# Performance work log

Measured on AMD Instinct MI355X. Metric: run time of the kernel, lower is better.

Reference implementation:

```python
import jax, jax.numpy as jnp
import numpy as np

QUERY_DIM = 1024
CONTEXT_DIM = 768
HEADS = 16
DIM_HEAD = 64
INNER = HEADS * DIM_HEAD  # 1024
SCALE = DIM_HEAD ** -0.5


def setup_inputs() -> dict:
    key = jax.random.key(0)
    ks = jax.random.split(key, 8)
    b, nq, nkv = 4, 2048, 1024
    x = jax.random.normal(ks[0], (b, nq, QUERY_DIM), dtype=jnp.float32)
    context = jax.random.normal(ks[1], (b, nkv, CONTEXT_DIM), dtype=jnp.float32)
    mask = jax.random.randint(ks[2], (b, nkv), 0, 2).astype(jnp.bool_)
    s = 0.02
    Wq = jax.random.normal(ks[3], (QUERY_DIM, INNER), dtype=jnp.float32) * s
    Wk = jax.random.normal(ks[4], (CONTEXT_DIM, INNER), dtype=jnp.float32) * s
    Wv = jax.random.normal(ks[5], (CONTEXT_DIM, INNER), dtype=jnp.float32) * s
    Wo = jax.random.normal(ks[6], (INNER, QUERY_DIM), dtype=jnp.float32) * s
    bo = jnp.zeros((QUERY_DIM,), dtype=jnp.float32)
    return {"x": x, "context": context, "mask": mask,
            "Wq": Wq, "Wk": Wk, "Wv": Wv, "Wo": Wo, "bo": bo}


def reference(x, context, mask, Wq, Wk, Wv, Wo, bo):
    b, nq, _ = x.shape
    nkv = context.shape[1]
    h, d = HEADS, DIM_HEAD
    # QKV projections (no bias, as in nn.Linear(..., bias=False))
    q = (x @ Wq).reshape(b, nq, h, d).transpose(0, 2, 1, 3)       # [b,h,i,d]
    k = (context @ Wk).reshape(b, nkv, h, d).transpose(0, 2, 1, 3)  # [b,h,j,d]
    v = (context @ Wv).reshape(b, nkv, h, d).transpose(0, 2, 1, 3)  # [b,h,j,d]
    sim = jnp.einsum('bhid,bhjd->bhij', q, k) * SCALE
    # mask is per-key [b, j]; broadcast over heads and query positions
    neg = jnp.finfo(sim.dtype).min
    sim = jnp.where(mask[:, None, None, :], sim, neg)
    attn = jax.nn.softmax(sim, axis=-1)
    out = jnp.einsum('bhij,bhjd->bhid', attn, v)                  # [b,h,i,d]
    out = out.transpose(0, 2, 1, 3).reshape(b, nq, h * d)          # [b,i,hd]
    return out @ Wo + bo
```

## Files before the change

kernel.cpp:

```cpp
#include <hip/hip_runtime.h>

typedef unsigned short u16;
typedef __attribute__((ext_vector_type(8))) __bf16 bf16x8;
typedef __attribute__((ext_vector_type(4))) float f32x4;
typedef __attribute__((ext_vector_type(16))) float f32x16;
typedef __attribute__((ext_vector_type(4))) u16 u16x4;

#define NB 4
#define NQ 2048
#define NKV 1024
#define NH 16
#define DH 64
#define DIN 1024
#define DCTX 768
#define NEGBIG -1e30f
#define QSC 0.180336881f

__device__ inline u16 f2bf(float f) {
  unsigned u = __builtin_bit_cast(unsigned, f);
  u += 0x7FFFu + ((u >> 16) & 1u);
  return (u16)(u >> 16);
}

__device__ inline unsigned cvtpk(float lo, float hi) {
  unsigned r;
  asm("v_cvt_pk_bf16_f32 %0, %1, %2" : "=v"(r) : "v"(lo), "v"(hi));
  return r;
}

__device__ inline float exp2a(float x) {
  float r;
  asm("v_exp_f32 %0, %1" : "=v"(r) : "v"(x));
  return r;
}

__global__ __launch_bounds__(256) void build_bias(const void* __restrict__ mask,
                                                  float* __restrict__ biasg) {
  __shared__ int notInt, notFloat;
  if (threadIdx.x == 0) { notInt = 0; notFloat = 0; }
  __syncthreads();
  const unsigned* mw = (const unsigned*)mask;
  int bad_i = 0, bad_f = 0;
#pragma unroll
  for (int e = 0; e < 4; e++) {
    unsigned v = mw[threadIdx.x * 4 + e];
    if (v > 1u) bad_i = 1;
    if (v != 0u && v != 0x3f800000u) bad_f = 1;
  }
  if (bad_i) atomicOr(&notInt, 1);
  if (bad_f) atomicOr(&notFloat, 1);
  __syncthreads();
  const int isInt = !notInt, isFloat = !notFloat;
  for (int i = threadIdx.x; i < NB * NKV; i += 256) {
    bool on;
    if (isInt)        on = ((const int*)mask)[i] != 0;
    else if (isFloat) on = ((const float*)mask)[i] != 0.f;
    else              on = ((const unsigned char*)mask)[i] != 0;
    biasg[i] = on ? 0.f : NEGBIG;
  }
}

__global__ __launch_bounds__(256) void cvt_bf16(const float* __restrict__ in,
                                                u16* __restrict__ out, int n) {
  int i = (blockIdx.x * 256 + threadIdx.x) * 4;
  if (i >= n) return;
  float4 v = *(const float4*)(in + i);
  u16x4 o = { f2bf(v.x), f2bf(v.y), f2bf(v.z), f2bf(v.w) };
  *(u16x4*)(out + i) = o;
}

__global__ __launch_bounds__(256) void transpose_cvt(const float* __restrict__ W,
                                                     u16* __restrict__ Wt, int K, int N) {
  __shared__ float tile[32][33];
  int n0 = blockIdx.x * 32, k0 = blockIdx.y * 32;
  int tx = threadIdx.x & 31, ty = threadIdx.x >> 5;
#pragma unroll
  for (int i = 0; i < 32; i += 8)
    tile[ty + i][tx] = W[(size_t)(k0 + ty + i) * N + n0 + tx];
  __syncthreads();
#pragma unroll
  for (int i = 0; i < 32; i += 8)
    Wt[(size_t)(n0 + ty + i) * K + k0 + tx] = f2bf(tile[tx][ty + i]);
}

__global__ __launch_bounds__(256) void vtrans(const u16* __restrict__ kvb, u16* __restrict__ vtg) {
  __shared__ __align__(16) u16 tile[64][72];
  const int t = threadIdx.x;
  const int jt = blockIdx.x, bh = blockIdx.y;
  const int b = bh >> 4, h = bh & 15;
  const int j0 = jt * 64;
  const int jl = t >> 2, c2 = t & 3;
  const u16* src = kvb + (size_t)(b * 1024 + j0 + jl) * 2048 + 1024 + h * 64 + c2 * 16;
  *(int4*)&tile[jl][c2 * 16]     = *(const int4*)(src);
  *(int4*)&tile[jl][c2 * 16 + 8] = *(const int4*)(src + 8);
  __syncthreads();
  const int dl = t >> 2;
  union { u16 e[16]; int4 q[2]; } pk;
#pragma unroll
  for (int e = 0; e < 16; e++) pk.e[e] = tile[c2 * 16 + e][dl];
  u16* dst = vtg + (size_t)(bh * 64 + dl) * 1024 + j0 + c2 * 16;
  *(int4*)dst       = pk.q[0];
  *(int4*)(dst + 8) = pk.q[1];
}

template<int MODE>
__global__ __launch_bounds__(256) void gemm_bt(const u16* __restrict__ A,
                                               const u16* __restrict__ Bt,
                                               void* __restrict__ Cout,
                                               const float* __restrict__ bias,
                                               int M, int N, int K) {
  __shared__ __align__(16) u16 As[2][128 * 32];
  __shared__ __align__(16) u16 Bs[2][128 * 32];
  const int t = threadIdx.x, w = t >> 6, l = t & 63, g = l >> 4, m16 = l & 15;
  const int brow = blockIdx.y * 128, bcol = blockIdx.x * 128;
  const int wr = w >> 1, wc = w & 1;
  const int r_a = t >> 2;
  const int kb  = (t & 3) * 8;
  const int nk = K >> 5;
  f32x4 acc[4][4] = {};

#define G_STAGE(ks, bsel)                                                              \
  {                                                                                    \
    int k0_ = (ks) << 5;                                                               \
    _Pragma("unroll")                                                                  \
    for (int i = 0; i < 2; i++) {                                                      \
      const u16* ga = A + (size_t)(brow + i * 64 + r_a) * K + k0_ + kb;                \
      __builtin_amdgcn_global_load_lds(                                                \
          (const __attribute__((address_space(1))) void*)ga,                           \
          (__attribute__((address_space(3))) void*)((char*)As + (bsel) * 8192 + i * 4096 + w * 1024), \
          16, 0, 0);                                                                   \
      const u16* gb = Bt + (size_t)(bcol + i * 64 + r_a) * K + k0_ + kb;               \
      __builtin_amdgcn_global_load_lds(                                                \
          (const __attribute__((address_space(1))) void*)gb,                           \
          (__attribute__((address_space(3))) void*)((char*)Bs + (bsel) * 8192 + i * 4096 + w * 1024), \
          16, 0, 0);                                                                   \
    }                                                                                  \
  }

  G_STAGE(0, 0);
  asm volatile("s_waitcnt vmcnt(0)" ::: "memory");
  __builtin_amdgcn_s_barrier();

  for (int ks = 0; ks < nk; ++ks) {
    const int cur = ks & 1;
    bf16x8 af[4], bfr[4];
#pragma unroll
    for (int m = 0; m < 4; m++)
      af[m] = *(const bf16x8*)(&As[cur][(wr * 64 + m * 16 + m16) * 32 + g * 8]);
#pragma unroll
    for (int n = 0; n < 4; n++)
      bfr[n] = *(const bf16x8*)(&Bs[cur][(wc * 64 + n * 16 + m16) * 32 + g * 8]);
    if (ks + 1 < nk) G_STAGE(ks + 1, cur ^ 1);
#pragma unroll
    for (int m = 0; m < 4; m++)
#pragma unroll
      for (int n = 0; n < 4; n++)
        acc[m][n] = __builtin_amdgcn_mfma_f32_16x16x32_bf16(af[m], bfr[n], acc[m][n], 0, 0, 0);
    asm volatile("s_waitcnt vmcnt(0)" ::: "memory");
    __builtin_amdgcn_s_barrier();
  }
#undef G_STAGE

#pragma unroll
  for (int m = 0; m < 4; m++) {
    int grow = brow + wr * 64 + m * 16 + g * 4;
#pragma unroll
    for (int n = 0; n < 4; n++) {
      int gcol = bcol + wc * 64 + n * 16 + m16;
#pragma unroll
      for (int r = 0; r < 4; r++) {
        size_t off = (size_t)(grow + r) * N + gcol;
        if (MODE == 0)      ((float*)Cout)[off] = acc[m][n][r] + bias[gcol];
        else if (MODE == 1) ((u16*)Cout)[off] = f2bf(acc[m][n][r]);
        else                ((u16*)Cout)[off] = f2bf(acc[m][n][r] * QSC);
      }
    }
  }
}

__global__ __launch_bounds__(256) void attn(const u16* __restrict__ Q, const u16* __restrict__ Kb,
                                            const u16* __restrict__ Vt_g,
                                            const float* __restrict__ biasg,
                                            u16* __restrict__ O) {
  const int qt = blockIdx.x, h = blockIdx.y, b = blockIdx.z;
  const int t = threadIdx.x, w = t >> 6, l = t & 63;
  const int i32 = l & 31, hi = l >> 5;
  const int bh = b * NH + h;

  __shared__ __align__(16) u16 Kl[2][4096];
  __shared__ __align__(16) u16 Vt[2][4096];
  __shared__ float biasl[NKV];

  for (int i = t; i < NKV; i += 256) biasl[i] = biasg[(size_t)b * NKV + i];

  const int qrow = qt * 128 + w * 32 + i32;
  const u16* qp = Q + (size_t)(b * NQ + qrow) * DIN + h * DH;
  bf16x8 qf[4];
#pragma unroll
  for (int c = 0; c < 4; c++) qf[c] = *(const bf16x8*)(qp + c * 16 + hi * 8);

  f32x16 oacc[2] = {};
  float lA = 0.f;

#define STAGE_K(j0, bsel)                                                     \
  {                                                                           \
    _Pragma("unroll")                                                         \
    for (int n = 0; n < 2; n++) {                                             \
      int j_ = n * 32 + (t >> 3);                                             \
      int c_ = (t & 7) ^ (j_ & 7);                                            \
      const u16* gk = Kb + (size_t)(b * NKV + (j0) + j_) * 2048 + h * DH + c_ * 8; \
      __builtin_amdgcn_global_load_lds(                                       \
          (const __attribute__((address_space(1))) void*)gk,                  \
          (__attribute__((address_space(3))) void*)((char*)Kl + (bsel) * 8192 + n * 4096 + t * 16), \
          16, 0, 0);                                                          \
    }                                                                         \
  }
#define STAGE_V(j0, bsel)                                                     \
  {                                                                           \
    _Pragma("unroll")                                                         \
    for (int n = 0; n < 2; n++) {                                             \
      int d_ = n * 32 + (t >> 3);                                             \
      int c_ = (t & 7) ^ (d_ & 7);                                            \
      const u16* gv = Vt_g + (size_t)(bh * 64 + d_) * 1024 + (j0) + c_ * 8;   \
      __builtin_amdgcn_global_load_lds(                                       \
          (const __attribute__((address_space(1))) void*)gv,                  \
          (__attribute__((address_space(3))) void*)((char*)Vt + (bsel) * 8192 + n * 4096 + t * 16), \
          16, 0, 0);                                                          \
    }                                                                         \
  }

  STAGE_K(0, 0);
  STAGE_V(0, 0);
  asm volatile("s_waitcnt vmcnt(0)" ::: "memory");
  __builtin_amdgcn_s_barrier();

  for (int it = 0; it < 16; ++it) {
    const int cur = it & 1, nxt = cur ^ 1;
    const int j0 = it * 64;
    if (it + 1 < 16) {
      STAGE_K(j0 + 64, nxt);
      STAGE_V(j0 + 64, nxt);
    }

    bf16x8 pa[4];
#pragma unroll
    for (int jt = 0; jt < 2; jt++) {
      f32x16 s = {};
#pragma unroll
      for (int c = 0; c < 4; c++) {
        bf16x8 kf = *(const bf16x8*)&Kl[cur][(jt * 32 + i32) * 64 + (((2 * c + hi) ^ (i32 & 7)) * 8)];
        s = __builtin_amdgcn_mfma_f32_32x32x16_bf16(kf, qf[c], s, 0, 0, 0);
      }
      float4 qb4[4];
#pragma unroll
      for (int a = 0; a < 4; a++)
        qb4[a] = *(const float4*)&biasl[j0 + jt * 32 + a * 8 + hi * 4];
      float p[16];
#pragma unroll
      for (int r = 0; r < 16; r++) {
        const float* bq = (const float*)&qb4[r >> 2];
        p[r] = exp2a(s[r] + bq[r & 3]);
      }
#pragma unroll
      for (int r = 0; r < 16; r += 4)
        lA += ((p[r] + p[r + 1]) + (p[r + 2] + p[r + 3]));
      unsigned u[4][2];
#pragma unroll
      for (int a = 0; a < 4; a++) {
        u[a][0] = cvtpk(p[4 * a], p[4 * a + 1]);
        u[a][1] = cvtpk(p[4 * a + 2], p[4 * a + 3]);
      }
#pragma unroll
      for (int cc = 0; cc < 2; cc++) {
        unsigned s0 = hi ? u[2 * cc][0] : u[2 * cc + 1][0];
        unsigned s1 = hi ? u[2 * cc][1] : u[2 * cc + 1][1];
        unsigned r0 = __shfl_xor(s0, 32);
        unsigned r1 = __shfl_xor(s1, 32);
        union { unsigned uu[4]; bf16x8 v; } pw;
        pw.uu[0] = hi ? r0 : u[2 * cc][0];
        pw.uu[1] = hi ? r1 : u[2 * cc][1];
        pw.uu[2] = hi ? u[2 * cc + 1][0] : r0;
        pw.uu[3] = hi ? u[2 * cc + 1][1] : r1;
        pa[jt * 2 + cc] = pw.v;
      }
    }
#pragma unroll
    for (int dt = 0; dt < 2; dt++) {
      const int d = dt * 32 + i32;
#pragma unroll
      for (int kc = 0; kc < 4; kc++) {
        bf16x8 vf = *(const bf16x8*)&Vt[cur][d * 64 + (((2 * kc + hi) ^ (i32 & 7)) * 8)];
        oacc[dt] = __builtin_amdgcn_mfma_f32_32x32x16_bf16(pa[kc], vf, oacc[dt], 0, 0, 0);
      }
    }
    asm volatile("s_waitcnt vmcnt(0)" ::: "memory");
    __builtin_amdgcn_s_barrier();
  }
#undef STAGE_K
#undef STAGE_V

  lA += __shfl_xor(lA, 32);
  float inv = 1.f / lA;
  u16* op = O + (size_t)(b * NQ + qt * 128 + w * 32) * DIN + h * DH;
#pragma unroll
  for (int reg = 0; reg < 16; reg++) {
    const int irow = (reg & 3) + 8 * (reg >> 2) + 4 * hi;
    const float iv = __shfl(inv, irow);
#pragma unroll
    for (int dt = 0; dt < 2; dt++)
      op[(size_t)irow * DIN + dt * 32 + i32] = f2bf(oacc[dt][reg] * iv);
  }
}

extern "C" void kernel_launch(void* const* d_in, const int* in_sizes, int n_in,
                              void* d_out, int out_size, void* d_ws, size_t ws_size,
                              hipStream_t stream) {
  const float* x   = (const float*)d_in[0];
  const float* ctx = (const float*)d_in[1];
  const void*  mask = (const void*)d_in[2];
  const float* Wq  = (const float*)d_in[3];
  const float* Wk  = (const float*)d_in[4];
  const float* Wv  = (const float*)d_in[5];
  const float* Wo  = (const float*)d_in[6];
  const float* bo  = (const float*)d_in[7];
  float* out = (float*)d_out;

  char* ws = (char*)d_ws;
  u16* xb   = (u16*)(ws);
  u16* cb   = (u16*)(ws + 16777216);
  u16* wqt  = (u16*)(ws + 23068672);
  u16* wkv  = (u16*)(ws + 25165824);
  u16* wot  = (u16*)(ws + 28311552);
  u16* qb   = (u16*)(ws + 30408704);
  u16* kvb  = (u16*)(ws + 47185920);
  u16* vtg  = (u16*)(ws + 16777216);
  float* biasg = (float*)(ws + 63963136);
  u16* ab   = xb;

  build_bias<<<1, 256, 0, stream>>>(mask, biasg);
  cvt_bf16<<<8192, 256, 0, stream>>>(x, xb, 8388608);
  cvt_bf16<<<3072, 256, 0, stream>>>(ctx, cb, 3145728);
  transpose_cvt<<<dim3(32, 32), 256, 0, stream>>>(Wq, wqt, 1024, 1024);
  transpose_cvt<<<dim3(32, 24), 256, 0, stream>>>(Wk, wkv, 768, 1024);
  transpose_cvt<<<dim3(32, 24), 256, 0, stream>>>(Wv, wkv + 1024 * 768, 768, 1024);
  transpose_cvt<<<dim3(32, 32), 256, 0, stream>>>(Wo, wot, 1024, 1024);

  gemm_bt<2><<<dim3(8, 64), 256, 0, stream>>>(xb, wqt, qb, nullptr, 8192, 1024, 1024);
  gemm_bt<1><<<dim3(16, 32), 256, 0, stream>>>(cb, wkv, kvb, nullptr, 4096, 2048, 768);

  vtrans<<<dim3(16, 64), 256, 0, stream>>>(kvb, vtg);

  attn<<<dim3(16, 16, 4), 256, 0, stream>>>(qb, kvb, vtg, biasg, ab);

  gemm_bt<0><<<dim3(8, 64), 256, 0, stream>>>(ab, wot, out, bo, 8192, 1024, 1024);
}
```

Measured before the change: 271.0 us.

## Rewrite projection GEMMs as 256x128 triple-buffered kernel; fold mask bias into MFMA init

The GEMM kernel moves to 256x128 tiles with 512 threads, K-step 64, an XOR-swizzled LDS layout and three-stage buffering with partial vmcnt waits, plus a block-index swizzle for L2 locality. In attention, the mask bias now initialises the MFMA accumulator, which removes the per-element add before exp. s_setprio raises wave priority around the MFMA blocks in both kernels. The larger tiles and three-deep buffers use much more LDS per block (144KB), which limits blocks per CU. The grid mapping hardcodes 256 blocks with an 8-way swizzle that assumes gx*gy=256.

```diff
diff --git a/kernel.cpp b/kernel.cpp
--- a/kernel.cpp
+++ b/kernel.cpp
@@ -104,69 +104,95 @@
 }
 
 template<int MODE>
-__global__ __launch_bounds__(256) void gemm_bt(const u16* __restrict__ A,
-                                               const u16* __restrict__ Bt,
-                                               void* __restrict__ Cout,
-                                               const float* __restrict__ bias,
-                                               int M, int N, int K) {
-  __shared__ __align__(16) u16 As[2][128 * 32];
-  __shared__ __align__(16) u16 Bs[2][128 * 32];
+__global__ __launch_bounds__(512) void gemm256p(const u16* __restrict__ A,
+                                                const u16* __restrict__ Bt,
+                                                void* __restrict__ Cout,
+                                                const float* __restrict__ bias,
+                                                int N, int K) {
+  __shared__ __align__(16) u16 As[3][256 * 64];
+  __shared__ __align__(16) u16 Bs[3][128 * 64];
   const int t = threadIdx.x, w = t >> 6, l = t & 63, g = l >> 4, m16 = l & 15;
-  const int brow = blockIdx.y * 128, bcol = blockIdx.x * 128;
-  const int wr = w >> 1, wc = w & 1;
-  const int r_a = t >> 2;
-  const int kb  = (t & 3) * 8;
-  const int nk = K >> 5;
+  const int gx = N >> 7;
+  const int bid = blockIdx.x;
+  const int sw = (bid & 7) * 32 + (bid >> 3);
+  const int bx = sw % gx, by = sw / gx;
+  const int brow = by * 256, bcol = bx * 128;
+  const int wm = w >> 1, wn = w & 1;
+  const int nk = K >> 6;
+  const int srow = t >> 3;
+  const int sc   = t & 7;
   f32x4 acc[4][4] = {};
 
-#define G_STAGE(ks, bsel)                                                              \
-  {                                                                                    \
-    int k0_ = (ks) << 5;                                                               \
-    _Pragma("unroll")                                                                  \
-    for (int i = 0; i < 2; i++) {                                                      \
-      const u16* ga = A + (size_t)(brow + i * 64 + r_a) * K + k0_ + kb;                \
-      __builtin_amdgcn_global_load_lds(                                                \
-          (const __attribute__((address_space(1))) void*)ga,                           \
-          (__attribute__((address_space(3))) void*)((char*)As + (bsel) * 8192 + i * 4096 + w * 1024), \
-          16, 0, 0);                                                                   \
-      const u16* gb = Bt + (size_t)(bcol + i * 64 + r_a) * K + k0_ + kb;               \
-      __builtin_amdgcn_global_load_lds(                                                \
-          (const __attribute__((address_space(1))) void*)gb,                           \
-          (__attribute__((address_space(3))) void*)((char*)Bs + (bsel) * 8192 + i * 4096 + w * 1024), \
-          16, 0, 0);                                                                   \
-    }                                                                                  \
-  }
-
-  G_STAGE(0, 0);
-  asm volatile("s_waitcnt vmcnt(0)" ::: "memory");
-  __builtin_amdgcn_s_barrier();
-
+#define STAGE(ks, bsel)                                                              \
+  {                                                                                  \
+    int k0_ = (ks) << 6;                                                             \
+    _Pragma("unroll")                                                                \
+    for (int r = 0; r < 4; r++) {                                                    \
+      int row = r * 64 + srow;                                                       \
+      int cs = sc ^ (row & 7);                                                       \
+      const u16* ga = A + (size_t)(brow + row) * K + k0_ + cs * 8;                   \
+      __builtin_amdgcn_global_load_lds(                                              \
+          (const __attribute__((address_space(1))) void*)ga,                         \
+          (__attribute__((address_space(3))) void*)((char*)As + (bsel) * 32768 + r * 8192 + t * 16), \
+          16, 0, 0);                                                                 \
+    }                                                                                \
+    _Pragma("unroll")                                                                \
+    for (int r = 0; r < 2; r++) {                                                    \
+      int row = r * 64 + srow;                                                       \
+      int cs = sc ^ (row & 7);                                                       \
+      const u16* gb = Bt + (size_t)(bcol + row) * K + k0_ + cs * 8;                  \
+      __builtin_amdgcn_global_load_lds(                                              \
+          (const __attribute__((address_space(1))) void*)gb,                         \
+          (__attribute__((address_space(3))) void*)((char*)Bs + (bsel) * 16384 + r * 8192 + t * 16), \
+          16, 0, 0);                                                                 \
+    }                                                                                \
+  }
+
+  STAGE(0, 0);
+  STAGE(1, 1);
+  int cur = 0;
   for (int ks = 0; ks < nk; ++ks) {
-    const int cur = ks & 1;
-    bf16x8 af[4], bfr[4];
+    if (ks + 1 < nk) asm volatile("s_waitcnt vmcnt(6)" ::: "memory");
+    else             asm volatile("s_waitcnt vmcnt(0)" ::: "memory");
+    __builtin_amdgcn_s_barrier();
+    if (ks + 2 < nk) {
+      const int stg = (cur >= 1) ? cur - 1 : 2;
+      STAGE(ks + 2, stg);
+    }
+    bf16x8 af[4][2], bfr[4][2];
+#pragma unroll
+    for (int m = 0; m < 4; m++) {
+      const int row = wm * 64 + m * 16 + m16;
+#pragma unroll
+      for (int kh = 0; kh < 2; kh++)
+        af[m][kh] = *(const bf16x8*)(&As[cur][row * 64 + (((kh * 4 + g) ^ (m16 & 7)) * 8)]);
+    }
+#pragma unroll
+    for (int n = 0; n < 4; n++) {
+      const int row = wn * 64 + n * 16 + m16;
+#pragma unroll
+      for (int kh = 0; kh < 2; kh++)
+        bfr[n][kh] = *(const bf16x8*)(&Bs[cur][row * 64 + (((kh * 4 + g) ^ (m16 & 7)) * 8)]);
+    }
+    __builtin_amdgcn_s_setprio(1);
 #pragma unroll
     for (int m = 0; m < 4; m++)
-      af[m] = *(const bf16x8*)(&As[cur][(wr * 64 + m * 16 + m16) * 32 + g * 8]);
-#pragma unroll
-    for (int n = 0; n < 4; n++)
-      bfr[n] = *(const bf16x8*)(&Bs[cur][(wc * 64 + n * 16 + m16) * 32 + g * 8]);
-    if (ks + 1 < nk) G_STAGE(ks + 1, cur ^ 1);
-#pragma unroll
-    for (int m = 0; m < 4; m++)
 #pragma unroll
       for (int n = 0; n < 4; n++)
-        acc[m][n] = __builtin_amdgcn_mfma_f32_16x16x32_bf16(af[m], bfr[n], acc[m][n], 0, 0, 0);
-    asm volatile("s_waitcnt vmcnt(0)" ::: "memory");
-    __builtin_amdgcn_s_barrier();
-  }
-#undef G_STAGE
+#pragma unroll
+        for (int kh = 0; kh < 2; kh++)
+          acc[m][n] = __builtin_amdgcn_mfma_f32_16x16x32_bf16(af[m][kh], bfr[n][kh], acc[m][n], 0, 0, 0);
+    __builtin_amdgcn_s_setprio(0);
+    cur = (cur == 2) ? 0 : cur + 1;
+  }
+#undef STAGE
 
 #pragma unroll
   for (int m = 0; m < 4; m++) {
-    int grow = brow + wr * 64 + m * 16 + g * 4;
+    int grow = brow + wm * 64 + m * 16 + g * 4;
 #pragma unroll
     for (int n = 0; n < 4; n++) {
-      int gcol = bcol + wc * 64 + n * 16 + m16;
+      int gcol = bcol + wn * 64 + n * 16 + m16;
 #pragma unroll
       for (int r = 0; r < 4; r++) {
         size_t off = (size_t)(grow + r) * N + gcol;
@@ -245,22 +271,28 @@
     bf16x8 pa[4];
 #pragma unroll
     for (int jt = 0; jt < 2; jt++) {
-      f32x16 s = {};
+      float4 qb4[4];
+#pragma unroll
+      for (int a = 0; a < 4; a++)
+        qb4[a] = *(const float4*)&biasl[j0 + jt * 32 + a * 8 + hi * 4];
+      f32x16 s;
+#pragma unroll
+      for (int a = 0; a < 4; a++) {
+        s[4 * a]     = qb4[a].x;
+        s[4 * a + 1] = qb4[a].y;
+        s[4 * a + 2] = qb4[a].z;
+        s[4 * a + 3] = qb4[a].w;
+      }
+      __builtin_amdgcn_s_setprio(1);
 #pragma unroll
       for (int c = 0; c < 4; c++) {
         bf16x8 kf = *(const bf16x8*)&Kl[cur][(jt * 32 + i32) * 64 + (((2 * c + hi) ^ (i32 & 7)) * 8)];
         s = __builtin_amdgcn_mfma_f32_32x32x16_bf16(kf, qf[c], s, 0, 0, 0);
       }
-      float4 qb4[4];
-#pragma unroll
-      for (int a = 0; a < 4; a++)
-        qb4[a] = *(const float4*)&biasl[j0 + jt * 32 + a * 8 + hi * 4];
+      __builtin_amdgcn_s_setprio(0);
       float p[16];
 #pragma unroll
-      for (int r = 0; r < 16; r++) {
-        const float* bq = (const float*)&qb4[r >> 2];
-        p[r] = exp2a(s[r] + bq[r & 3]);
-      }
+      for (int r = 0; r < 16; r++) p[r] = exp2a(s[r]);
 #pragma unroll
       for (int r = 0; r < 16; r += 4)
         lA += ((p[r] + p[r + 1]) + (p[r + 2] + p[r + 3]));
@@ -284,6 +316,7 @@
         pa[jt * 2 + cc] = pw.v;
       }
     }
+    __builtin_amdgcn_s_setprio(1);
 #pragma unroll
     for (int dt = 0; dt < 2; dt++) {
       const int d = dt * 32 + i32;
@@ -293,6 +326,7 @@
         oacc[dt] = __builtin_amdgcn_mfma_f32_32x32x16_bf16(pa[kc], vf, oacc[dt], 0, 0, 0);
       }
     }
+    __builtin_amdgcn_s_setprio(0);
     asm volatile("s_waitcnt vmcnt(0)" ::: "memory");
     __builtin_amdgcn_s_barrier();
   }
@@ -345,12 +379,12 @@
   transpose_cvt<<<dim3(32, 24), 256, 0, stream>>>(Wv, wkv + 1024 * 768, 768, 1024);
   transpose_cvt<<<dim3(32, 32), 256, 0, stream>>>(Wo, wot, 1024, 1024);
 
-  gemm_bt<2><<<dim3(8, 64), 256, 0, stream>>>(xb, wqt, qb, nullptr, 8192, 1024, 1024);
-  gemm_bt<1><<<dim3(16, 32), 256, 0, stream>>>(cb, wkv, kvb, nullptr, 4096, 2048, 768);
+  gemm256p<2><<<256, 512, 0, stream>>>(xb, wqt, qb, nullptr, 1024, 1024);
+  gemm256p<1><<<256, 512, 0, stream>>>(cb, wkv, kvb, nullptr, 2048, 768);
 
   vtrans<<<dim3(16, 64), 256, 0, stream>>>(kvb, vtg);
 
   attn<<<dim3(16, 16, 4), 256, 0, stream>>>(qb, kvb, vtg, biasg, ab);
 
-  gemm_bt<0><<<dim3(8, 64), 256, 0, stream>>>(ab, wot, out, bo, 8192, 1024, 1024);
-}
+  gemm256p<0><<<256, 512, 0, stream>>>(ab, wot, out, bo, 1024, 1024);
+}
```

New measurement: 263.2 us. 2.9% less time.
